# Performance work log

Hardware: AMD Instinct MI355X
Metric: run time of the kernel (lower is better)

## Reference

```python
import jax, jax.numpy as jnp
from jax import lax
import numpy as np

T, D, H, E, K = 4096, 1024, 2048, 8, 2

def setup_inputs() -> dict:
    key = jax.random.key(0)
    ks = jax.random.split(key, 5)
    x = jax.random.normal(ks[0], (T, D), dtype=jnp.float32)
    weights = jax.random.uniform(ks[1], (T, K), dtype=jnp.float32)
    indices = jax.random.randint(ks[2], (T, K), 0, E, dtype=jnp.int64)
    # GatedMLP params (bias=False): fc1 weight [2H, D], fc2 weight [D, H], stacked over experts
    W1 = jax.random.normal(ks[3], (E, 2 * H, D), dtype=jnp.float32) * 0.02
    W2 = jax.random.normal(ks[4], (E, D, H), dtype=jnp.float32) * 0.02
    return {"x": x, "weights": weights, "indices": indices, "W1": W1, "W2": W2}

def reference(x, weights, indices, W1, W2):
    # Combine per-token routing weights into a per-(token, expert) weight matrix.
    # Tokens not routed to expert e get weight 0, so the dense per-expert GatedMLP
    # weighted-sum is mathematically identical to the gather->MLP->scatter-add loop.
    onehot = jax.nn.one_hot(indices, E, dtype=weights.dtype)        # [T, K, E]
    w_te = jnp.einsum('tke,tk->et', onehot, weights)                # [E, T]

    def body(y, carry):
        W1e, W2e, we = carry                                        # [2H,D], [D,H], [T]
        h = x @ W1e.T                                               # [T, 2H]
        u, gate = jnp.split(h, 2, axis=-1)                          # [T, H] each
        out = (u * jax.nn.silu(gate)) @ W2e.T                       # [T, D]
        return y + out * we[:, None], None

    y, _ = lax.scan(body, jnp.zeros_like(x), (W1, W2, w_te))
    return y
```

## Files before the change

kernel.cpp:

```cpp
#include <hip/hip_runtime.h>
#include <stdint.h>

#define T_TOK 4096
#define D_DIM 1024
#define H_DIM 2048
#define E_EXP 8
#define K_TOP 2
#define NTK   (T_TOK * K_TOP)
#define MAX_TILES 80

typedef short bf16x8 __attribute__((ext_vector_type(8)));
typedef float f32x4  __attribute__((ext_vector_type(4)));

#define MINI(a, b) ((a) < (b) ? (a) : (b))

__device__ __forceinline__ unsigned short f2bf(float f) {
  unsigned u = __float_as_uint(f);
  u += 0x7fffu + ((u >> 16) & 1u);
  return (unsigned short)(u >> 16);
}

#define GLDS16(gp, lp)                                                        \
  __builtin_amdgcn_global_load_lds(                                           \
      (const __attribute__((address_space(1))) void*)(gp),                    \
      (__attribute__((address_space(3))) void*)(lp), 16, 0, 0)


__global__ __launch_bounds__(256) void k_route1(const int* __restrict__ idx,
                                                int* __restrict__ meta) {
  __shared__ int lc[E_EXP];
  int tid = threadIdx.x;
  if (tid < E_EXP) lc[tid] = 0;
  __syncthreads();
  for (int i = tid; i < NTK; i += 256) atomicAdd(&lc[idx[i] & (E_EXP - 1)], 1);
  __syncthreads();
  if (tid == 0) {
    int off = 0, nt = 0;
    for (int e = 0; e < E_EXP; ++e) {
      int c = lc[e];
      meta[0 + e]  = c;
      meta[8 + e]  = off;
      meta[16 + e] = off;
      for (int r = 0; r < c; r += 128) {
        meta[32 + nt]  = e;
        meta[112 + nt] = off + r;
        meta[192 + nt] = MINI(128, c - r);
        ++nt;
      }
      off += c;
    }
    meta[24] = nt;
  }
}

__global__ __launch_bounds__(256) void k_route2(const int* __restrict__ idx,
                                                const float* __restrict__ w,
                                                int* __restrict__ meta,
                                                int* __restrict__ rows,
                                                float* __restrict__ wv) {
  int i = blockIdx.x * 256 + threadIdx.x;
  if (i < NTK) {
    int e = idx[i] & (E_EXP - 1);
    int p = atomicAdd(&meta[16 + e], 1);
    rows[p] = i >> 1;
    wv[p]   = w[i];
  }
}

__global__ __launch_bounds__(256) void k_cvt(const float* __restrict__ src,
                                             unsigned short* __restrict__ dst,
                                             int n4) {
  int i = blockIdx.x * 256 + threadIdx.x;
  if (i < n4) {
    float4 v = ((const float4*)src)[i];
    ushort4 o;
    o.x = f2bf(v.x); o.y = f2bf(v.y); o.z = f2bf(v.z); o.w = f2bf(v.w);
    ((ushort4*)dst)[i] = o;
  }
}

__global__ __launch_bounds__(128, 2) void k_gemm1(
    const unsigned short* __restrict__ xb,
    const unsigned short* __restrict__ W1b,
    const int* __restrict__ meta,
    const int* __restrict__ rows,
    const float* __restrict__ wv,
    unsigned short* __restrict__ act) {
  int nt = meta[24];
  int tb = blockIdx.x;
  if (tb >= nt) return;
  int e     = meta[32 + tb];
  int r0    = meta[112 + tb];
  int valid = meta[192 + tb];
  int n0    = blockIdx.y * 64;

  __shared__ unsigned short lA[128 * 64];
  __shared__ unsigned short lB1[64 * 64];
  __shared__ unsigned short lB2[64 * 64];
  __shared__ float sw[128];

  int tid = threadIdx.x;
  int wave = tid >> 6, lane = tid & 63;

  sw[tid] = wv[r0 + MINI(tid, valid - 1)];

  const unsigned short* w1e = W1b + (size_t)e * (4096 * 1024);

  const unsigned short *pA[8], *pB1[4], *pB2[4];
#pragma unroll
  for (int it = 0; it < 8; ++it) {
    int c = it * 128 + tid;
    int r = c >> 3, cc = c & 7;
    int g = cc ^ (r & 7);
    int tok = rows[r0 + MINI(r, valid - 1)];
    pA[it] = xb + (size_t)tok * 1024 + g * 8;
  }
#pragma unroll
  for (int it = 0; it < 4; ++it) {
    int c = it * 128 + tid;
    int r = c >> 3, cc = c & 7;
    int g = cc ^ (r & 7);
    pB1[it] = w1e + (size_t)(n0 + r) * 1024 + g * 8;
    pB2[it] = w1e + (size_t)(2048 + n0 + r) * 1024 + g * 8;
  }

  f32x4 zero = {0.f, 0.f, 0.f, 0.f};
  f32x4 au[4][4], ag[4][4];
#pragma unroll
  for (int i = 0; i < 4; ++i)
#pragma unroll
    for (int j = 0; j < 4; ++j) { au[i][j] = zero; ag[i][j] = zero; }

  int mb = wave * 64;
  int fr = lane & 15, q = lane >> 4;

  for (int k0 = 0; k0 < 1024; k0 += 64) {
    __syncthreads();
#pragma unroll
    for (int it = 0; it < 8; ++it)
      GLDS16(pA[it] + k0, &lA[(it * 128 + wave * 64) * 8]);
#pragma unroll
    for (int it = 0; it < 4; ++it) {
      int lb = (it * 128 + wave * 64) * 8;
      GLDS16(pB1[it] + k0, &lB1[lb]);
      GLDS16(pB2[it] + k0, &lB2[lb]);
    }
    __syncthreads();
#pragma unroll
    for (int kk = 0; kk < 2; ++kk) {
      int co = (((kk << 2) + q) ^ (fr & 7)) * 8 + fr * 64;
      bf16x8 a[4];
#pragma unroll
      for (int i = 0; i < 4; ++i)
        a[i] = *(const bf16x8*)&lA[(mb + i * 16) * 64 + co];
#pragma unroll
      for (int j = 0; j < 4; ++j) {
        bf16x8 bu = *(const bf16x8*)&lB1[(j * 16) * 64 + co];
        bf16x8 bg = *(const bf16x8*)&lB2[(j * 16) * 64 + co];
#pragma unroll
        for (int i = 0; i < 4; ++i) {
          au[i][j] = __builtin_amdgcn_mfma_f32_16x16x32_bf16(a[i], bu, au[i][j], 0, 0, 0);
          ag[i][j] = __builtin_amdgcn_mfma_f32_16x16x32_bf16(a[i], bg, ag[i][j], 0, 0, 0);
        }
      }
    }
  }

#pragma unroll
  for (int i = 0; i < 4; ++i) {
#pragma unroll
    for (int reg = 0; reg < 4; ++reg) {
      int lm = mb + i * 16 + q * 4 + reg;
      if (lm < valid) {
        float wrow = sw[lm];
        size_t orow = (size_t)(r0 + lm) * 2048;
#pragma unroll
        for (int j = 0; j < 4; ++j) {
          float u = au[i][j][reg];
          float g = ag[i][j][reg];
          float s = g / (1.f + __expf(-g));
          act[orow + (n0 + j * 16 + fr)] = f2bf(u * s * wrow);
        }
      }
    }
  }
}

__global__ __launch_bounds__(128, 2) void k_gemm2(
    const unsigned short* __restrict__ act,
    const unsigned short* __restrict__ W2b,
    const int* __restrict__ meta,
    const int* __restrict__ rows,
    float* __restrict__ out) {
  int nt = meta[24];
  int tb = blockIdx.x;
  if (tb >= nt) return;
  int e     = meta[32 + tb];
  int r0    = meta[112 + tb];
  int valid = meta[192 + tb];
  int n0    = blockIdx.y * 128;

  __shared__ unsigned short lA[128 * 64];
  __shared__ unsigned short lB[128 * 64];
  __shared__ int st[128];

  int tid = threadIdx.x;
  int wave = tid >> 6, lane = tid & 63;
  st[tid] = rows[r0 + MINI(tid, valid - 1)];

  const unsigned short* w2e = W2b + (size_t)e * (1024 * 2048);

  const unsigned short *pA[8], *pB[8];
#pragma unroll
  for (int it = 0; it < 8; ++it) {
    int c = it * 128 + tid;
    int r = c >> 3, cc = c & 7;
    int g = cc ^ (r & 7);
    pA[it] = act + (size_t)(r0 + MINI(r, valid - 1)) * 2048 + g * 8;
    pB[it] = w2e + (size_t)(n0 + r) * 2048 + g * 8;
  }

  f32x4 zero = {0.f, 0.f, 0.f, 0.f};
  f32x4 acc[4][8];
#pragma unroll
  for (int i = 0; i < 4; ++i)
#pragma unroll
    for (int j = 0; j < 8; ++j) acc[i][j] = zero;

  int mb = wave * 64;
  int fr = lane & 15, q = lane >> 4;

  for (int k0 = 0; k0 < 2048; k0 += 64) {
    __syncthreads();
#pragma unroll
    for (int it = 0; it < 8; ++it) {
      int lb = (it * 128 + wave * 64) * 8;
      GLDS16(pA[it] + k0, &lA[lb]);
      GLDS16(pB[it] + k0, &lB[lb]);
    }
    __syncthreads();
#pragma unroll
    for (int kk = 0; kk < 2; ++kk) {
      int co = (((kk << 2) + q) ^ (fr & 7)) * 8 + fr * 64;
      bf16x8 a[4];
#pragma unroll
      for (int i = 0; i < 4; ++i)
        a[i] = *(const bf16x8*)&lA[(mb + i * 16) * 64 + co];
#pragma unroll
      for (int j = 0; j < 8; ++j) {
        bf16x8 b = *(const bf16x8*)&lB[(j * 16) * 64 + co];
#pragma unroll
        for (int i = 0; i < 4; ++i)
          acc[i][j] = __builtin_amdgcn_mfma_f32_16x16x32_bf16(a[i], b, acc[i][j], 0, 0, 0);
      }
    }
  }

#pragma unroll
  for (int i = 0; i < 4; ++i) {
#pragma unroll
    for (int reg = 0; reg < 4; ++reg) {
      int lm = mb + i * 16 + q * 4 + reg;
      if (lm < valid) {
        int tok = st[lm];
        float* op = out + (size_t)tok * 1024;
#pragma unroll
        for (int j = 0; j < 8; ++j)
          atomicAdd(&op[n0 + j * 16 + fr], acc[i][j][reg]);
      }
    }
  }
}

extern "C" void kernel_launch(void* const* d_in, const int* in_sizes, int n_in,
                              void* d_out, int out_size, void* d_ws, size_t ws_size,
                              hipStream_t stream) {
  const float* x  = (const float*)d_in[0];
  const float* w  = (const float*)d_in[1];
  const int*  idx = (const int*)d_in[2];
  const float* W1 = (const float*)d_in[3];
  const float* W2 = (const float*)d_in[4];
  float* out = (float*)d_out;

  char* ws = (char*)d_ws;
  unsigned short* W1b = (unsigned short*)(ws);
  unsigned short* W2b = (unsigned short*)(ws + 67108864);
  unsigned short* xb  = (unsigned short*)(ws + 100663296);
  unsigned short* act = (unsigned short*)(ws + 109051904);
  int*   rows = (int*)(ws + 142606336);
  float* wv   = (float*)(ws + 142639104);
  int*   meta = (int*)(ws + 142671872);

  hipMemsetAsync(d_out, 0, (size_t)out_size * sizeof(float), stream);

  k_route1<<<1, 256, 0, stream>>>(idx, meta);
  k_route2<<<(NTK + 255) / 256, 256, 0, stream>>>(idx, w, meta, rows, wv);

  k_cvt<<<(T_TOK * D_DIM / 4 + 255) / 256, 256, 0, stream>>>(x, xb, T_TOK * D_DIM / 4);
  k_cvt<<<(E_EXP * 2 * H_DIM * D_DIM / 4 + 255) / 256, 256, 0, stream>>>(W1, W1b, E_EXP * 2 * H_DIM * D_DIM / 4);
  k_cvt<<<(E_EXP * D_DIM * H_DIM / 4 + 255) / 256, 256, 0, stream>>>(W2, W2b, E_EXP * D_DIM * H_DIM / 4);

  dim3 g1(MAX_TILES, H_DIM / 64);
  dim3 g2(MAX_TILES, D_DIM / 128);
  k_gemm1<<<g1, 128, 0, stream>>>(xb, W1b, meta, rows, wv, act);
  k_gemm2<<<g2, 128, 0, stream>>>(act, W2b, meta, rows, out);
}
```

Baseline: 498.1 us.

## Double M-tile to 256 rows with 4 waves; fuse routing and conversion kernels

The grouped GEMM tiles grow from 128 to 256 token rows, and each block now runs 256 threads (4 waves), so every W1/W2 tile loaded into LDS is reused across twice as many tokens and weight traffic per token drops. The two routing kernels merge into one single-block kernel that scatters rows using an LDS cursor, and the three fp32-to-bf16 conversions merge into one launch to cut launch overhead. In exchange, per-expert tail tiles have more padding waste, there are fewer blocks to fill the CUs, and scattering 8192 entries from one block is serial work.

```diff
diff --git a/kernel.cpp b/kernel.cpp
--- a/kernel.cpp
+++ b/kernel.cpp
@@ -7,7 +7,7 @@
 #define E_EXP 8
 #define K_TOP 2
 #define NTK   (T_TOK * K_TOP)
-#define MAX_TILES 80
+#define MAX_TILES 48
 
 typedef short bf16x8 __attribute__((ext_vector_type(8)));
 typedef float f32x4  __attribute__((ext_vector_type(4)));
@@ -26,9 +26,13 @@
       (__attribute__((address_space(3))) void*)(lp), 16, 0, 0)
 
 
-__global__ __launch_bounds__(256) void k_route1(const int* __restrict__ idx,
-                                                int* __restrict__ meta) {
+__global__ __launch_bounds__(256) void k_route(const int* __restrict__ idx,
+                                               const float* __restrict__ w,
+                                               int* __restrict__ meta,
+                                               int* __restrict__ rows,
+                                               float* __restrict__ wv) {
   __shared__ int lc[E_EXP];
+  __shared__ int lcur[E_EXP];
   int tid = threadIdx.x;
   if (tid < E_EXP) lc[tid] = 0;
   __syncthreads();
@@ -38,48 +42,57 @@
     int off = 0, nt = 0;
     for (int e = 0; e < E_EXP; ++e) {
       int c = lc[e];
-      meta[0 + e]  = c;
-      meta[8 + e]  = off;
-      meta[16 + e] = off;
-      for (int r = 0; r < c; r += 128) {
+      meta[0 + e] = c;
+      meta[8 + e] = off;
+      lcur[e] = off;
+      for (int r = 0; r < c; r += 256) {
         meta[32 + nt]  = e;
         meta[112 + nt] = off + r;
-        meta[192 + nt] = MINI(128, c - r);
+        meta[192 + nt] = MINI(256, c - r);
         ++nt;
       }
       off += c;
     }
     meta[24] = nt;
   }
-}
-
-__global__ __launch_bounds__(256) void k_route2(const int* __restrict__ idx,
-                                                const float* __restrict__ w,
-                                                int* __restrict__ meta,
-                                                int* __restrict__ rows,
-                                                float* __restrict__ wv) {
-  int i = blockIdx.x * 256 + threadIdx.x;
-  if (i < NTK) {
+  __syncthreads();
+  for (int i = tid; i < NTK; i += 256) {
     int e = idx[i] & (E_EXP - 1);
-    int p = atomicAdd(&meta[16 + e], 1);
+    int p = atomicAdd(&lcur[e], 1);
     rows[p] = i >> 1;
     wv[p]   = w[i];
   }
 }
 
-__global__ __launch_bounds__(256) void k_cvt(const float* __restrict__ src,
-                                             unsigned short* __restrict__ dst,
-                                             int n4) {
-  int i = blockIdx.x * 256 + threadIdx.x;
-  if (i < n4) {
-    float4 v = ((const float4*)src)[i];
-    ushort4 o;
-    o.x = f2bf(v.x); o.y = f2bf(v.y); o.z = f2bf(v.z); o.w = f2bf(v.w);
-    ((ushort4*)dst)[i] = o;
-  }
-}
-
-__global__ __launch_bounds__(128, 2) void k_gemm1(
+#define NX4  (T_TOK * D_DIM / 4)
+#define NW14 (E_EXP * 2 * H_DIM * D_DIM / 4)
+#define NW24 (E_EXP * D_DIM * H_DIM / 4)
+#define NCVT (NX4 + NW14 + NW24)
+
+__global__ __launch_bounds__(256) void k_cvt3(const float* __restrict__ x,
+                                              const float* __restrict__ W1,
+                                              const float* __restrict__ W2,
+                                              unsigned short* __restrict__ xb,
+                                              unsigned short* __restrict__ W1b,
+                                              unsigned short* __restrict__ W2b) {
+  int gid = blockIdx.x * 256 + threadIdx.x;
+  const float* src;
+  unsigned short* dst;
+  int i;
+  if (gid < NX4) {
+    src = x; dst = xb; i = gid;
+  } else if (gid < NX4 + NW14) {
+    src = W1; dst = W1b; i = gid - NX4;
+  } else if (gid < NCVT) {
+    src = W2; dst = W2b; i = gid - (NX4 + NW14);
+  } else return;
+  float4 v = ((const float4*)src)[i];
+  ushort4 o;
+  o.x = f2bf(v.x); o.y = f2bf(v.y); o.z = f2bf(v.z); o.w = f2bf(v.w);
+  ((ushort4*)dst)[i] = o;
+}
+
+__global__ __launch_bounds__(256, 2) void k_gemm1(
     const unsigned short* __restrict__ xb,
     const unsigned short* __restrict__ W1b,
     const int* __restrict__ meta,
@@ -94,10 +107,10 @@
   int valid = meta[192 + tb];
   int n0    = blockIdx.y * 64;
 
-  __shared__ unsigned short lA[128 * 64];
+  __shared__ unsigned short lA[256 * 64];
   __shared__ unsigned short lB1[64 * 64];
   __shared__ unsigned short lB2[64 * 64];
-  __shared__ float sw[128];
+  __shared__ float sw[256];
 
   int tid = threadIdx.x;
   int wave = tid >> 6, lane = tid & 63;
@@ -106,18 +119,18 @@
 
   const unsigned short* w1e = W1b + (size_t)e * (4096 * 1024);
 
-  const unsigned short *pA[8], *pB1[4], *pB2[4];
+  const unsigned short *pA[8], *pB1[2], *pB2[2];
 #pragma unroll
   for (int it = 0; it < 8; ++it) {
-    int c = it * 128 + tid;
+    int c = it * 256 + tid;
     int r = c >> 3, cc = c & 7;
     int g = cc ^ (r & 7);
     int tok = rows[r0 + MINI(r, valid - 1)];
     pA[it] = xb + (size_t)tok * 1024 + g * 8;
   }
 #pragma unroll
-  for (int it = 0; it < 4; ++it) {
-    int c = it * 128 + tid;
+  for (int it = 0; it < 2; ++it) {
+    int c = it * 256 + tid;
     int r = c >> 3, cc = c & 7;
     int g = cc ^ (r & 7);
     pB1[it] = w1e + (size_t)(n0 + r) * 1024 + g * 8;
@@ -138,10 +151,10 @@
     __syncthreads();
 #pragma unroll
     for (int it = 0; it < 8; ++it)
-      GLDS16(pA[it] + k0, &lA[(it * 128 + wave * 64) * 8]);
-#pragma unroll
-    for (int it = 0; it < 4; ++it) {
-      int lb = (it * 128 + wave * 64) * 8;
+      GLDS16(pA[it] + k0, &lA[(it * 256 + wave * 64) * 8]);
+#pragma unroll
+    for (int it = 0; it < 2; ++it) {
+      int lb = (it * 256 + wave * 64) * 8;
       GLDS16(pB1[it] + k0, &lB1[lb]);
       GLDS16(pB2[it] + k0, &lB2[lb]);
     }
@@ -186,7 +199,7 @@
   }
 }
 
-__global__ __launch_bounds__(128, 2) void k_gemm2(
+__global__ __launch_bounds__(256, 2) void k_gemm2(
     const unsigned short* __restrict__ act,
     const unsigned short* __restrict__ W2b,
     const int* __restrict__ meta,
@@ -200,9 +213,9 @@
   int valid = meta[192 + tb];
   int n0    = blockIdx.y * 128;
 
-  __shared__ unsigned short lA[128 * 64];
+  __shared__ unsigned short lA[256 * 64];
   __shared__ unsigned short lB[128 * 64];
-  __shared__ int st[128];
+  __shared__ int st[256];
 
   int tid = threadIdx.x;
   int wave = tid >> 6, lane = tid & 63;
@@ -210,13 +223,19 @@
 
   const unsigned short* w2e = W2b + (size_t)e * (1024 * 2048);
 
-  const unsigned short *pA[8], *pB[8];
+  const unsigned short *pA[8], *pB[4];
 #pragma unroll
   for (int it = 0; it < 8; ++it) {
-    int c = it * 128 + tid;
+    int c = it * 256 + tid;
     int r = c >> 3, cc = c & 7;
     int g = cc ^ (r & 7);
     pA[it] = act + (size_t)(r0 + MINI(r, valid - 1)) * 2048 + g * 8;
+  }
+#pragma unroll
+  for (int it = 0; it < 4; ++it) {
+    int c = it * 256 + tid;
+    int r = c >> 3, cc = c & 7;
+    int g = cc ^ (r & 7);
     pB[it] = w2e + (size_t)(n0 + r) * 2048 + g * 8;
   }
 
@@ -233,11 +252,11 @@
   for (int k0 = 0; k0 < 2048; k0 += 64) {
     __syncthreads();
 #pragma unroll
-    for (int it = 0; it < 8; ++it) {
-      int lb = (it * 128 + wave * 64) * 8;
-      GLDS16(pA[it] + k0, &lA[lb]);
-      GLDS16(pB[it] + k0, &lB[lb]);
-    }
+    for (int it = 0; it < 8; ++it)
+      GLDS16(pA[it] + k0, &lA[(it * 256 + wave * 64) * 8]);
+#pragma unroll
+    for (int it = 0; it < 4; ++it)
+      GLDS16(pB[it] + k0, &lB[(it * 256 + wave * 64) * 8]);
     __syncthreads();
 #pragma unroll
     for (int kk = 0; kk < 2; ++kk) {
@@ -293,15 +312,11 @@
 
   hipMemsetAsync(d_out, 0, (size_t)out_size * sizeof(float), stream);
 
-  k_route1<<<1, 256, 0, stream>>>(idx, meta);
-  k_route2<<<(NTK + 255) / 256, 256, 0, stream>>>(idx, w, meta, rows, wv);
-
-  k_cvt<<<(T_TOK * D_DIM / 4 + 255) / 256, 256, 0, stream>>>(x, xb, T_TOK * D_DIM / 4);
-  k_cvt<<<(E_EXP * 2 * H_DIM * D_DIM / 4 + 255) / 256, 256, 0, stream>>>(W1, W1b, E_EXP * 2 * H_DIM * D_DIM / 4);
-  k_cvt<<<(E_EXP * D_DIM * H_DIM / 4 + 255) / 256, 256, 0, stream>>>(W2, W2b, E_EXP * D_DIM * H_DIM / 4);
+  k_route<<<1, 256, 0, stream>>>(idx, w, meta, rows, wv);
+  k_cvt3<<<(NCVT + 255) / 256, 256, 0, stream>>>(x, W1, W2, xb, W1b, W2b);
 
   dim3 g1(MAX_TILES, H_DIM / 64);
   dim3 g2(MAX_TILES, D_DIM / 128);
-  k_gemm1<<<g1, 128, 0, stream>>>(xb, W1b, meta, rows, wv, act);
-  k_gemm2<<<g2, 128, 0, stream>>>(act, W2b, meta, rows, out);
-}
+  k_gemm1<<<g1, 256, 0, stream>>>(xb, W1b, meta, rows, wv, act);
+  k_gemm2<<<g2, 256, 0, stream>>>(act, W2b, meta, rows, out);
+}
```

New measurement: 461.9 us. 1.08x faster.
